# Kernel optimization log

Hardware: AMD Instinct MI355X
Metric: run time of the kernel (lower is better)

The kernel has to match this reference:

```python
import jax, jax.numpy as jnp
import numpy as np

D = 256   # vec_dim
H = 8     # head_num
P = 1024  # patch_num
N = 8     # batch


def setup_inputs() -> dict:
    key = jax.random.key(0)
    ks = jax.random.split(key, 11)
    s = 0.05
    return {
        "inputs": jax.random.normal(ks[0], (N, D, P), dtype=jnp.float32),
        "pos_mat": jax.random.normal(ks[1], (1, H, P, P), dtype=jnp.float32),
        "Wk": jax.random.normal(ks[2], (H * D, D), dtype=jnp.float32) * s,
        "bk": jax.random.normal(ks[3], (H * D,), dtype=jnp.float32) * s,
        "Wq": jax.random.normal(ks[4], (H * D, D), dtype=jnp.float32) * s,
        "bq": jax.random.normal(ks[5], (H * D,), dtype=jnp.float32) * s,
        "Wv": jax.random.normal(ks[6], (H * D, D), dtype=jnp.float32) * s,
        "bv": jax.random.normal(ks[7], (H * D,), dtype=jnp.float32) * s,
        "Wo": jax.random.normal(ks[8], (D, H * D), dtype=jnp.float32) * s,
        "bo": jax.random.normal(ks[9], (D,), dtype=jnp.float32) * s,
    }


def reference(inputs, pos_mat, Wk, bk, Wq, bq, Wv, bv, Wo, bo):
    n, d, p = inputs.shape  # [N, D, P]
    h = Wk.shape[0] // d
    # 1x1 Conv1d == per-position GEMM: [H*D,D] x [N,D,P] -> [N,H*D,P] -> [N,H,D,P]
    k = (jnp.einsum('od,ndp->nop', Wk, inputs) + bk[:, None]).reshape(n, h, d, p)
    q = (jnp.einsum('od,ndp->nop', Wq, inputs) + bq[:, None]).reshape(n, h, d, p)
    v = (jnp.einsum('od,ndp->nop', Wv, inputs) + bv[:, None]).reshape(n, h, d, p)
    # attn[n,h,kpos,qpos] = K^T Q / sqrt(D), shape [N,H,P,P]
    attn = jnp.einsum('nhdk,nhdq->nhkq', k, q) / jnp.sqrt(jnp.asarray(d, inputs.dtype))
    attn = attn + pos_mat
    # NOTE: original uses Softmax(dim=2), i.e. over the KEY axis, not the last dim
    w = jax.nn.softmax(attn, axis=2)
    out = jnp.einsum('nhdk,nhkq->nhdq', v, w).reshape(n, h * d, p)
    return jnp.einsum('oi,nip->nop', Wo, out) + bo[:, None]
```

## Files before the change

kernel.cpp:

```cpp
#include <hip/hip_runtime.h>

typedef __bf16 bf16;
typedef __attribute__((ext_vector_type(8))) __bf16 bf16x8;
typedef __attribute__((ext_vector_type(4))) __bf16 bf16x4;
typedef __attribute__((ext_vector_type(2))) __bf16 bf16x2;
typedef __attribute__((ext_vector_type(4))) float f32x4;

#define MFMA16(a, b, c) __builtin_amdgcn_mfma_f32_16x16x32_bf16(a, b, c, 0, 0, 0)

__device__ __forceinline__ void gload_lds16(const void* g, void* l) {
  __builtin_amdgcn_global_load_lds(
      (const __attribute__((address_space(1))) void*)g,
      (__attribute__((address_space(3))) void*)l, 16, 0, 0);
}

constexpr int NH = 8, DD = 256, PP = 1024;

constexpr size_t WB_YT  = 33554432;
constexpr size_t WB_XB  = 67108864;
constexpr size_t WB_XBT = 71303168;
constexpr size_t WB_MB  = 75497472;
constexpr size_t WB_UB  = 76546048;
constexpr size_t WB_U   = 77594624;
constexpr size_t WB_BP  = 77602816;

constexpr int FL_PT0  = 0;
constexpr int FL_XT0  = 16384;
constexpr int FL_LRED = 0;
constexpr int FL_SZ   = 81920;

#define EXP_SHIFT 4.0f

__global__ __launch_bounds__(256, 1) void msa_mu(
    const float* __restrict__ Wk, const float* __restrict__ Wq,
    const float* __restrict__ Wo, const float* __restrict__ Wv,
    bf16* __restrict__ Mb, bf16* __restrict__ Ub) {
  __shared__ float lds[64 * 65];
  const int t = threadIdx.x;
  const int i0 = (blockIdx.x >> 1) * 64;
  const int jh = blockIdx.x & 1;
  const int h = blockIdx.y;
  const int mode = blockIdx.z;
  const int j0 = (t & 63) * 2 + jh * 128;
  const int ihalf = t >> 6;
  float acc0[16], acc1[16];
#pragma unroll
  for (int r = 0; r < 16; ++r) { acc0[r] = 0.f; acc1[r] = 0.f; }
  const float* __restrict__ W2 = (mode == 0) ? Wq : Wv;
  for (int dhc = 0; dhc < 256; dhc += 64) {
    __syncthreads();
    if (mode == 0) {
#pragma unroll
      for (int s = 0; s < 16; ++s) {
        int f = t + s * 256;
        int dh = f >> 6, ii = f & 63;
        lds[dh * 65 + ii] = Wk[(h * 256 + dhc + dh) * 256 + i0 + ii];
      }
    } else {
#pragma unroll
      for (int s = 0; s < 16; ++s) {
        int f = t + s * 256;
        int oo = f >> 6, dh = f & 63;
        lds[dh * 65 + oo] = Wo[(i0 + oo) * 2048 + h * 256 + dhc + dh];
      }
    }
    __syncthreads();
    for (int dl = 0; dl < 64; ++dl) {
      float2 wv = *reinterpret_cast<const float2*>(&W2[(h * 256 + dhc + dl) * 256 + j0]);
#pragma unroll
      for (int r = 0; r < 16; ++r) {
        float x = lds[dl * 65 + ihalf * 16 + r];
        acc0[r] = fmaf(x, wv.x, acc0[r]);
        acc1[r] = fmaf(x, wv.y, acc1[r]);
      }
    }
  }
  if (mode == 0) {
#pragma unroll
    for (int r = 0; r < 16; ++r) {
      int i = i0 + ihalf * 16 + r;
      bf16x2 v = { (__bf16)(acc0[r] * 0.0625f), (__bf16)(acc1[r] * 0.0625f) };
      *reinterpret_cast<bf16x2*>(&Mb[h * 65536 + i * 256 + j0]) = v;
    }
  } else {
#pragma unroll
    for (int r = 0; r < 16; ++r) {
      int o = i0 + ihalf * 16 + r;
      bf16x2 v = { (__bf16)acc0[r], (__bf16)acc1[r] };
      *reinterpret_cast<bf16x2*>(&Ub[o * 2048 + h * 256 + j0]) = v;
    }
  }
}

__global__ void msa_u(const float* __restrict__ Wk, const float* __restrict__ bq,
                      float* __restrict__ u) {
  __shared__ float bqs[256];
  const int h = blockIdx.x, t = threadIdx.x;
  bqs[t] = bq[h * 256 + t];
  __syncthreads();
  float acc = 0.f;
  for (int dh = 0; dh < 256; ++dh)
    acc = fmaf(Wk[(h * 256 + dh) * 256 + t], bqs[dh], acc);
  u[h * 256 + t] = acc * 0.0625f;
}

__global__ void msa_bp(const float* __restrict__ Wo, const float* __restrict__ bv,
                       const float* __restrict__ bo, float* __restrict__ bp) {
  const int o = blockIdx.x, t = threadIdx.x;
  float acc = 0.f;
  for (int f = t; f < 2048; f += 256)
    acc = fmaf(Wo[o * 2048 + f], bv[f], acc);
#pragma unroll
  for (int m = 32; m >= 1; m >>= 1) acc += __shfl_down(acc, m);
  __shared__ float part[4];
  if ((t & 63) == 0) part[t >> 6] = acc;
  __syncthreads();
  if (t == 0) bp[o] = bo[o] + part[0] + part[1] + part[2] + part[3];
}

__global__ __launch_bounds__(256, 4) void msa_cvtX(
    const float* __restrict__ X, bf16* __restrict__ Xb, bf16* __restrict__ XbT) {
  __shared__ __bf16 tl[64 * 68];
  const int t = threadIdx.x;
  const int p0 = blockIdx.x * 64, d0 = blockIdx.y * 64, n = blockIdx.z;
  const float* __restrict__ Xn = X + (size_t)n * DD * PP;
#pragma unroll
  for (int rr = 0; rr < 4; ++rr) {
    int r = (t >> 4) + rr * 16, c = (t & 15) * 4;
    float4 v = *reinterpret_cast<const float4*>(Xn + (size_t)(d0 + r) * PP + p0 + c);
    bf16x4 pk = { (__bf16)v.x, (__bf16)v.y, (__bf16)v.z, (__bf16)v.w };
    *reinterpret_cast<bf16x4*>(Xb + (size_t)n * DD * PP + (size_t)(d0 + r) * PP + p0 + c) = pk;
    *reinterpret_cast<bf16x4*>(&tl[r * 68 + c]) = pk;
  }
  __syncthreads();
#pragma unroll
  for (int rr = 0; rr < 4; ++rr) {
    int pr = (t >> 4) + rr * 16, dc = (t & 15) * 4;
    bf16x4 pk = { tl[(dc + 0) * 68 + pr], tl[(dc + 1) * 68 + pr],
                  tl[(dc + 2) * 68 + pr], tl[(dc + 3) * 68 + pr] };
    *reinterpret_cast<bf16x4*>(XbT + (size_t)n * PP * DD + (size_t)(p0 + pr) * DD + d0 + dc) = pk;
  }
}

__global__ __launch_bounds__(256, 2) void msa_flash(
    const bf16* __restrict__ XbT, const bf16* __restrict__ Xb,
    const bf16* __restrict__ Mb, const float* __restrict__ u,
    const float* __restrict__ pos, bf16* __restrict__ Yt) {
  extern __shared__ char smc[];
  const int t = threadIdx.x;
  const int lane = t & 63, w = t >> 6;
  const int g = lane >> 4, ln = lane & 15;
  const int kw = w >> 1, qw = w & 1;
  const int qt = blockIdx.x, h = blockIdx.y, n = blockIdx.z;
  const int qg0 = qt * 64, nh = n * 8 + h;
  const bf16* __restrict__ XbTn = XbT + (size_t)n * (PP * DD);
  const bf16* __restrict__ Xbn  = Xb + (size_t)n * (DD * PP);
  const bf16* __restrict__ Mh   = Mb + (size_t)h * (DD * DD);
  const float* __restrict__ posh = pos + (size_t)h * (PP * PP);
  float* lredp = (float*)(smc + FL_LRED);

  const int grl = lane >> 5;
  const int gcb = lane & 31;

  {
    bf16x8 ta[4][8];
#pragma unroll
    for (int mq = 0; mq < 4; ++mq)
#pragma unroll
      for (int s = 0; s < 8; ++s)
        ta[mq][s] = *reinterpret_cast<const bf16x8*>(
            XbTn + (size_t)(qg0 + mq * 16 + ln) * DD + s * 32 + g * 8);
#pragma unroll
    for (int ni = 0; ni < 4; ++ni) {
      const int i_ = w * 64 + ni * 16 + ln;
      bf16x8 tb8[8];
#pragma unroll
      for (int s = 0; s < 8; ++s)
        tb8[s] = *reinterpret_cast<const bf16x8*>(Mh + (size_t)i_ * DD + s * 32 + g * 8);
      const float uv = u[h * 256 + i_];
#pragma unroll
      for (int mq = 0; mq < 4; ++mq) {
        f32x4 acc = {0.f, 0.f, 0.f, 0.f};
#pragma unroll
        for (int s = 0; s < 8; ++s) acc = MFMA16(ta[mq][s], tb8[s], acc);
#pragma unroll
        for (int r = 0; r < 4; ++r) {
          const int q = mq * 16 + 4 * g + r;
          const int addr = FL_XT0 + q * 512 +
              (((w * 8 + ni * 2 + (ln >> 3)) ^ (q & 7)) << 4) + (ln & 7) * 2;
          *reinterpret_cast<__bf16*>(smc + addr) = (__bf16)(acc[r] + uv);
        }
      }
    }
  }
  __syncthreads();

  bf16x8 tb[2][8];
#pragma unroll
  for (int nq = 0; nq < 2; ++nq) {
    const int q_ = qw * 32 + nq * 16 + ln;
#pragma unroll
    for (int s = 0; s < 8; ++s)
      tb[nq][s] = *reinterpret_cast<const bf16x8*>(
          smc + FL_XT0 + q_ * 512 + (((4 * s + g) ^ (q_ & 7)) << 4));
  }
  __syncthreads();

#pragma unroll
  for (int c = 0; c < 8; ++c) {
    const int row = w * 16 + c * 2 + grl;
    const int cbg = gcb ^ (row & 7);
    gload_lds16(XbTn + (size_t)row * DD + cbg * 8,
                smc + FL_XT0 + w * 8192 + c * 1024);
  }
  __syncthreads();

  float lsum[2] = {0.f, 0.f};
  f32x4 yacc[4][4];
#pragma unroll
  for (int a = 0; a < 4; ++a)
#pragma unroll
    for (int b = 0; b < 4; ++b) { f32x4 z = {0.f, 0.f, 0.f, 0.f}; yacc[a][b] = z; }

  for (int kt = 0; kt < 16; ++kt) {
    const int kg0 = kt * 64;
    const int curXT = FL_XT0 + (kt & 1) * 32768;
    const int nxtXT = FL_XT0 + ((kt + 1) & 1) * 32768;
    const int curPT = FL_PT0 + (kt & 1) * 8192;
    if (kt < 15) {
#pragma unroll
      for (int c = 0; c < 8; ++c) {
        const int row = w * 16 + c * 2 + grl;
        const int cbg = gcb ^ (row & 7);
        gload_lds16(XbTn + (size_t)(kg0 + 64 + row) * DD + cbg * 8,
                    smc + nxtXT + w * 8192 + c * 1024);
      }
    }
    float posv[2][2][4];
#pragma unroll
    for (int mt = 0; mt < 2; ++mt)
#pragma unroll
      for (int nq = 0; nq < 2; ++nq) {
        const float* pr = posh + (size_t)(kg0 + kw * 32 + mt * 16 + 4 * g) * PP +
                          qg0 + qw * 32 + nq * 16 + ln;
#pragma unroll
        for (int r = 0; r < 4; ++r) posv[mt][nq][r] = pr[(size_t)r * PP];
      }
    f32x4 sacc[2][2];
#pragma unroll
    for (int a = 0; a < 2; ++a)
#pragma unroll
      for (int b = 0; b < 2; ++b) { f32x4 z = {0.f, 0.f, 0.f, 0.f}; sacc[a][b] = z; }
#pragma unroll
    for (int mt = 0; mt < 2; ++mt) {
      const int row = kw * 32 + mt * 16 + ln;
      bf16x8 af8[8];
#pragma unroll
      for (int s = 0; s < 8; ++s)
        af8[s] = *reinterpret_cast<const bf16x8*>(
            smc + curXT + row * 512 + (((4 * s + g) ^ (row & 7)) << 4));
#pragma unroll
      for (int s = 0; s < 8; ++s)
#pragma unroll
        for (int nq = 0; nq < 2; ++nq)
          sacc[mt][nq] = MFMA16(af8[s], tb[nq][s], sacc[mt][nq]);
    }
#pragma unroll
    for (int mt = 0; mt < 2; ++mt)
#pragma unroll
      for (int nq = 0; nq < 2; ++nq) {
        bf16x4 pk;
#pragma unroll
        for (int r = 0; r < 4; ++r) {
          float e = __expf(sacc[mt][nq][r] + posv[mt][nq][r] - EXP_SHIFT);
          lsum[nq] += e;
          pk[r] = (__bf16)e;
        }
        const int q_ = qw * 32 + nq * 16 + ln;
        *reinterpret_cast<bf16x4*>(smc + curPT + q_ * 128 +
            (((kw * 4 + mt * 2 + (g >> 1)) ^ (q_ & 7)) << 4) + ((g & 1) << 3)) = pk;
      }
    __syncthreads();
#pragma unroll
    for (int ks = 0; ks < 2; ++ks) {
      bf16x8 pa[4], xv[4];
#pragma unroll
      for (int mq = 0; mq < 4; ++mq) {
        const int q_ = mq * 16 + ln;
        pa[mq] = *reinterpret_cast<const bf16x8*>(
            smc + curPT + q_ * 128 + (((4 * ks + g) ^ (q_ & 7)) << 4));
      }
#pragma unroll
      for (int nd = 0; nd < 4; ++nd)
        xv[nd] = *reinterpret_cast<const bf16x8*>(
            Xbn + (size_t)(w * 64 + nd * 16 + ln) * PP + kg0 + ks * 32 + g * 8);
#pragma unroll
      for (int mq = 0; mq < 4; ++mq)
#pragma unroll
        for (int nd = 0; nd < 4; ++nd)
          yacc[mq][nd] = MFMA16(pa[mq], xv[nd], yacc[mq][nd]);
    }
  }

#pragma unroll
  for (int nq = 0; nq < 2; ++nq) {
    lsum[nq] += __shfl_xor(lsum[nq], 16);
    lsum[nq] += __shfl_xor(lsum[nq], 32);
  }
  if (lane < 16) {
#pragma unroll
    for (int nq = 0; nq < 2; ++nq)
      lredp[kw * 64 + qw * 32 + nq * 16 + ln] = lsum[nq];
  }
  __syncthreads();
  bf16* __restrict__ Ytp = Yt + (size_t)nh * (PP * DD);
#pragma unroll
  for (int mq = 0; mq < 4; ++mq) {
    f32x4 l0 = *reinterpret_cast<const f32x4*>(lredp + mq * 16 + 4 * g);
    f32x4 l1 = *reinterpret_cast<const f32x4*>(lredp + 64 + mq * 16 + 4 * g);
    f32x4 inv;
#pragma unroll
    for (int r = 0; r < 4; ++r) inv[r] = 1.0f / (l0[r] + l1[r]);
#pragma unroll
    for (int nd = 0; nd < 4; ++nd)
#pragma unroll
      for (int r = 0; r < 4; ++r)
        Ytp[(size_t)(qg0 + mq * 16 + 4 * g + r) * DD + w * 64 + nd * 16 + ln] =
            (__bf16)(yacc[mq][nd][r] * inv[r]);
  }
}

__global__ __launch_bounds__(256, 3) void msa_final4(
    const bf16* __restrict__ Ub, const bf16* __restrict__ Yt,
    const float* __restrict__ bp, float* __restrict__ out) {
  __shared__ char lsd[49152];
  const int t = threadIdx.x, lane = t & 63, w = t >> 6;
  const int g = lane >> 4, ln = lane & 15;
  const int pw = w & 1, ow = w >> 1;
  const int pb = blockIdx.x * 128, ob = blockIdx.y * 64, n = blockIdx.z;
  const bf16* __restrict__ Ytn = Yt + (size_t)n * 8 * (PP * DD);
  f32x4 acc[2][4];
#pragma unroll
  for (int a = 0; a < 2; ++a)
#pragma unroll
    for (int b = 0; b < 4; ++b) { f32x4 z = {0.f, 0.f, 0.f, 0.f}; acc[a][b] = z; }

  uint4 areg[2], breg[4];
  {
#pragma unroll
    for (int j = 0; j < 2; ++j) {
      int u_ = t + j * 256;
      areg[j] = *reinterpret_cast<const uint4*>(
          Ub + (size_t)(ob + (u_ >> 3)) * 2048 + 0 + (u_ & 7) * 8);
    }
#pragma unroll
    for (int j = 0; j < 4; ++j) {
      int v_ = t + j * 256;
      breg[j] = *reinterpret_cast<const uint4*>(
          Ytn + ((size_t)0 * PP + pb + (v_ >> 3)) * DD + 0 + (v_ & 7) * 8);
    }
#pragma unroll
    for (int j = 0; j < 2; ++j) {
      int u_ = t + j * 256, row = u_ >> 3, cb = u_ & 7;
      *reinterpret_cast<uint4*>(lsd + row * 128 + ((cb ^ (row & 7)) << 4)) = areg[j];
    }
#pragma unroll
    for (int j = 0; j < 4; ++j) {
      int v_ = t + j * 256, row = v_ >> 3, cb = v_ & 7;
      *reinterpret_cast<uint4*>(lsd + 8192 + row * 128 + ((cb ^ (row & 7)) << 4)) = breg[j];
    }
  }
  __syncthreads();

  for (int kc = 0; kc < 32; ++kc) {
    const int cur = (kc & 1) * 24576;
    const int nxt = ((kc + 1) & 1) * 24576;
    if (kc < 31) {
      const int k1 = (kc + 1) * 64, hh = k1 >> 8, dd = k1 & 255;
#pragma unroll
      for (int j = 0; j < 2; ++j) {
        int u_ = t + j * 256;
        areg[j] = *reinterpret_cast<const uint4*>(
            Ub + (size_t)(ob + (u_ >> 3)) * 2048 + k1 + (u_ & 7) * 8);
      }
#pragma unroll
      for (int j = 0; j < 4; ++j) {
        int v_ = t + j * 256;
        breg[j] = *reinterpret_cast<const uint4*>(
            Ytn + ((size_t)hh * PP + pb + (v_ >> 3)) * DD + dd + (v_ & 7) * 8);
      }
    }
#pragma unroll
    for (int ks = 0; ks < 2; ++ks) {
      bf16x8 a[2], b[4];
#pragma unroll
      for (int mo = 0; mo < 2; ++mo) {
        const int row = ow * 32 + mo * 16 + ln;
        a[mo] = *reinterpret_cast<const bf16x8*>(
            lsd + cur + row * 128 + (((4 * ks + g) ^ (row & 7)) << 4));
      }
#pragma unroll
      for (int np = 0; np < 4; ++np) {
        const int row = pw * 64 + np * 16 + ln;
        b[np] = *reinterpret_cast<const bf16x8*>(
            lsd + cur + 8192 + row * 128 + (((4 * ks + g) ^ (row & 7)) << 4));
      }
#pragma unroll
      for (int mo = 0; mo < 2; ++mo)
#pragma unroll
        for (int np = 0; np < 4; ++np) acc[mo][np] = MFMA16(a[mo], b[np], acc[mo][np]);
    }
    if (kc < 31) {
#pragma unroll
      for (int j = 0; j < 2; ++j) {
        int u_ = t + j * 256, row = u_ >> 3, cb = u_ & 7;
        *reinterpret_cast<uint4*>(lsd + nxt + row * 128 + ((cb ^ (row & 7)) << 4)) = areg[j];
      }
#pragma unroll
      for (int j = 0; j < 4; ++j) {
        int v_ = t + j * 256, row = v_ >> 3, cb = v_ & 7;
        *reinterpret_cast<uint4*>(lsd + nxt + 8192 + row * 128 + ((cb ^ (row & 7)) << 4)) = breg[j];
      }
    }
    __syncthreads();
  }

#pragma unroll
  for (int mo = 0; mo < 2; ++mo) {
    f32x4 bv = *reinterpret_cast<const f32x4*>(bp + ob + ow * 32 + mo * 16 + 4 * g);
#pragma unroll
    for (int np = 0; np < 4; ++np)
#pragma unroll
      for (int r = 0; r < 4; ++r) {
        const int o = ob + ow * 32 + mo * 16 + 4 * g + r;
        out[((size_t)n * DD + o) * PP + pb + pw * 64 + np * 16 + ln] =
            acc[mo][np][r] + bv[r];
      }
  }
}

extern "C" void kernel_launch(void* const* d_in, const int* in_sizes, int n_in,
                              void* d_out, int out_size, void* d_ws, size_t ws_size,
                              hipStream_t stream) {
  const float* X   = (const float*)d_in[0];
  const float* pos = (const float*)d_in[1];
  const float* Wk  = (const float*)d_in[2];
  const float* Wq  = (const float*)d_in[4];
  const float* bq  = (const float*)d_in[5];
  const float* Wv  = (const float*)d_in[6];
  const float* bv  = (const float*)d_in[7];
  const float* Wo  = (const float*)d_in[8];
  const float* bo  = (const float*)d_in[9];

  char* ws = (char*)d_ws;
  bf16* Yt  = (bf16*)(ws + WB_YT);
  bf16* Xb  = (bf16*)(ws + WB_XB);
  bf16* XbT = (bf16*)(ws + WB_XBT);
  bf16* Mb  = (bf16*)(ws + WB_MB);
  bf16* Ub  = (bf16*)(ws + WB_UB);
  float* u  = (float*)(ws + WB_U);
  float* bp = (float*)(ws + WB_BP);
  float* out = (float*)d_out;

  hipFuncSetAttribute(reinterpret_cast<const void*>(msa_flash),
                      hipFuncAttributeMaxDynamicSharedMemorySize, FL_SZ);

  msa_cvtX<<<dim3(16, 4, 8), 256, 0, stream>>>(X, Xb, XbT);
  msa_mu<<<dim3(8, 8, 2), 256, 0, stream>>>(Wk, Wq, Wo, Wv, Mb, Ub);
  msa_u<<<8, 256, 0, stream>>>(Wk, bq, u);
  msa_bp<<<256, 256, 0, stream>>>(Wo, bv, bo, bp);
  msa_flash<<<dim3(16, 8, 8), 256, FL_SZ, stream>>>(XbT, Xb, Mb, u, pos, Yt);
  msa_final4<<<dim3(8, 4, 8), 256, 0, stream>>>(Ub, Yt, bp, out);
}
```

Before: 282.5 us.

## Prefetch pos and X loads, add MFMA priority, remap flash grid, split msa_mu

Several separate changes ship together. In the flash kernel the pos_mat tile for the next key tile is prefetched into registers while the current tile computes, and the V-side X loads are hoisted to the top of each iteration. s_setprio raises wave priority around the MFMA blocks. The flash grid becomes 1D with heads innermost, so blocks sharing the same batch's X sit near each other in dispatch order and may reuse it in L2. msa_mu gets twice as many blocks with half the work each; the extra in-flight loads raise register pressure, which could limit the two-blocks-per-CU occupancy.

```diff
diff --git a/kernel.cpp b/kernel.cpp
--- a/kernel.cpp
+++ b/kernel.cpp
@@ -37,15 +37,15 @@
     bf16* __restrict__ Mb, bf16* __restrict__ Ub) {
   __shared__ float lds[64 * 65];
   const int t = threadIdx.x;
-  const int i0 = (blockIdx.x >> 1) * 64;
-  const int jh = blockIdx.x & 1;
+  const int i0 = (blockIdx.x >> 2) * 64;
+  const int jq = blockIdx.x & 3;
   const int h = blockIdx.y;
   const int mode = blockIdx.z;
-  const int j0 = (t & 63) * 2 + jh * 128;
-  const int ihalf = t >> 6;
-  float acc0[16], acc1[16];
-#pragma unroll
-  for (int r = 0; r < 16; ++r) { acc0[r] = 0.f; acc1[r] = 0.f; }
+  const int j0 = (t & 31) * 2 + jq * 64;
+  const int i8 = t >> 5;
+  float acc0[8], acc1[8];
+#pragma unroll
+  for (int r = 0; r < 8; ++r) { acc0[r] = 0.f; acc1[r] = 0.f; }
   const float* __restrict__ W2 = (mode == 0) ? Wq : Wv;
   for (int dhc = 0; dhc < 256; dhc += 64) {
     __syncthreads();
@@ -68,8 +68,8 @@
     for (int dl = 0; dl < 64; ++dl) {
       float2 wv = *reinterpret_cast<const float2*>(&W2[(h * 256 + dhc + dl) * 256 + j0]);
 #pragma unroll
-      for (int r = 0; r < 16; ++r) {
-        float x = lds[dl * 65 + ihalf * 16 + r];
+      for (int r = 0; r < 8; ++r) {
+        float x = lds[dl * 65 + i8 * 8 + r];
         acc0[r] = fmaf(x, wv.x, acc0[r]);
         acc1[r] = fmaf(x, wv.y, acc1[r]);
       }
@@ -77,15 +77,15 @@
   }
   if (mode == 0) {
 #pragma unroll
-    for (int r = 0; r < 16; ++r) {
-      int i = i0 + ihalf * 16 + r;
+    for (int r = 0; r < 8; ++r) {
+      int i = i0 + i8 * 8 + r;
       bf16x2 v = { (__bf16)(acc0[r] * 0.0625f), (__bf16)(acc1[r] * 0.0625f) };
       *reinterpret_cast<bf16x2*>(&Mb[h * 65536 + i * 256 + j0]) = v;
     }
   } else {
 #pragma unroll
-    for (int r = 0; r < 16; ++r) {
-      int o = i0 + ihalf * 16 + r;
+    for (int r = 0; r < 8; ++r) {
+      int o = i0 + i8 * 8 + r;
       bf16x2 v = { (__bf16)acc0[r], (__bf16)acc1[r] };
       *reinterpret_cast<bf16x2*>(&Ub[o * 2048 + h * 256 + j0]) = v;
     }
@@ -151,7 +151,8 @@
   const int lane = t & 63, w = t >> 6;
   const int g = lane >> 4, ln = lane & 15;
   const int kw = w >> 1, qw = w & 1;
-  const int qt = blockIdx.x, h = blockIdx.y, n = blockIdx.z;
+  const int bid = blockIdx.x;
+  const int h = bid & 7, qt = (bid >> 3) & 15, n = bid >> 7;
   const int qg0 = qt * 64, nh = n * 8 + h;
   const bf16* __restrict__ XbTn = XbT + (size_t)n * (PP * DD);
   const bf16* __restrict__ Xbn  = Xb + (size_t)n * (DD * PP);
@@ -213,6 +214,16 @@
     gload_lds16(XbTn + (size_t)row * DD + cbg * 8,
                 smc + FL_XT0 + w * 8192 + c * 1024);
   }
+  float posv[2][2][4];
+#pragma unroll
+  for (int mt = 0; mt < 2; ++mt)
+#pragma unroll
+    for (int nq = 0; nq < 2; ++nq) {
+      const float* pr = posh + (size_t)(kw * 32 + mt * 16 + 4 * g) * PP +
+                        qg0 + qw * 32 + nq * 16 + ln;
+#pragma unroll
+      for (int r = 0; r < 4; ++r) posv[mt][nq][r] = pr[(size_t)r * PP];
+    }
   __syncthreads();
 
   float lsum[2] = {0.f, 0.f};
@@ -236,21 +247,19 @@
                     smc + nxtXT + w * 8192 + c * 1024);
       }
     }
-    float posv[2][2][4];
-#pragma unroll
-    for (int mt = 0; mt < 2; ++mt)
-#pragma unroll
-      for (int nq = 0; nq < 2; ++nq) {
-        const float* pr = posh + (size_t)(kg0 + kw * 32 + mt * 16 + 4 * g) * PP +
-                          qg0 + qw * 32 + nq * 16 + ln;
-#pragma unroll
-        for (int r = 0; r < 4; ++r) posv[mt][nq][r] = pr[(size_t)r * PP];
-      }
+    bf16x8 xv[2][4];
+#pragma unroll
+    for (int ks = 0; ks < 2; ++ks)
+#pragma unroll
+      for (int nd = 0; nd < 4; ++nd)
+        xv[ks][nd] = *reinterpret_cast<const bf16x8*>(
+            Xbn + (size_t)(w * 64 + nd * 16 + ln) * PP + kg0 + ks * 32 + g * 8);
     f32x4 sacc[2][2];
 #pragma unroll
     for (int a = 0; a < 2; ++a)
 #pragma unroll
       for (int b = 0; b < 2; ++b) { f32x4 z = {0.f, 0.f, 0.f, 0.f}; sacc[a][b] = z; }
+    __builtin_amdgcn_s_setprio(1);
 #pragma unroll
     for (int mt = 0; mt < 2; ++mt) {
       const int row = kw * 32 + mt * 16 + ln;
@@ -264,6 +273,19 @@
 #pragma unroll
         for (int nq = 0; nq < 2; ++nq)
           sacc[mt][nq] = MFMA16(af8[s], tb[nq][s], sacc[mt][nq]);
+    }
+    __builtin_amdgcn_s_setprio(0);
+    float posvn[2][2][4];
+    if (kt < 15) {
+#pragma unroll
+      for (int mt = 0; mt < 2; ++mt)
+#pragma unroll
+        for (int nq = 0; nq < 2; ++nq) {
+          const float* pr = posh + (size_t)(kg0 + 64 + kw * 32 + mt * 16 + 4 * g) * PP +
+                            qg0 + qw * 32 + nq * 16 + ln;
+#pragma unroll
+          for (int r = 0; r < 4; ++r) posvn[mt][nq][r] = pr[(size_t)r * PP];
+        }
     }
 #pragma unroll
     for (int mt = 0; mt < 2; ++mt)
@@ -281,9 +303,10 @@
             (((kw * 4 + mt * 2 + (g >> 1)) ^ (q_ & 7)) << 4) + ((g & 1) << 3)) = pk;
       }
     __syncthreads();
+    __builtin_amdgcn_s_setprio(1);
 #pragma unroll
     for (int ks = 0; ks < 2; ++ks) {
-      bf16x8 pa[4], xv[4];
+      bf16x8 pa[4];
 #pragma unroll
       for (int mq = 0; mq < 4; ++mq) {
         const int q_ = mq * 16 + ln;
@@ -291,14 +314,19 @@
             smc + curPT + q_ * 128 + (((4 * ks + g) ^ (q_ & 7)) << 4));
       }
 #pragma unroll
-      for (int nd = 0; nd < 4; ++nd)
-        xv[nd] = *reinterpret_cast<const bf16x8*>(
-            Xbn + (size_t)(w * 64 + nd * 16 + ln) * PP + kg0 + ks * 32 + g * 8);
-#pragma unroll
       for (int mq = 0; mq < 4; ++mq)
 #pragma unroll
         for (int nd = 0; nd < 4; ++nd)
-          yacc[mq][nd] = MFMA16(pa[mq], xv[nd], yacc[mq][nd]);
+          yacc[mq][nd] = MFMA16(pa[mq], xv[ks][nd], yacc[mq][nd]);
+    }
+    __builtin_amdgcn_s_setprio(0);
+    if (kt < 15) {
+#pragma unroll
+      for (int mt = 0; mt < 2; ++mt)
+#pragma unroll
+        for (int nq = 0; nq < 2; ++nq)
+#pragma unroll
+          for (int r = 0; r < 4; ++r) posv[mt][nq][r] = posvn[mt][nq][r];
     }
   }
 
@@ -466,9 +494,9 @@
                       hipFuncAttributeMaxDynamicSharedMemorySize, FL_SZ);
 
   msa_cvtX<<<dim3(16, 4, 8), 256, 0, stream>>>(X, Xb, XbT);
-  msa_mu<<<dim3(8, 8, 2), 256, 0, stream>>>(Wk, Wq, Wo, Wv, Mb, Ub);
+  msa_mu<<<dim3(16, 8, 2), 256, 0, stream>>>(Wk, Wq, Wo, Wv, Mb, Ub);
   msa_u<<<8, 256, 0, stream>>>(Wk, bq, u);
   msa_bp<<<256, 256, 0, stream>>>(Wo, bv, bo, bp);
-  msa_flash<<<dim3(16, 8, 8), 256, FL_SZ, stream>>>(XbT, Xb, Mb, u, pos, Yt);
+  msa_flash<<<1024, 256, FL_SZ, stream>>>(XbT, Xb, Mb, u, pos, Yt);
   msa_final4<<<dim3(8, 4, 8), 256, 0, stream>>>(Ub, Yt, bp, out);
 }
```

New measurement: 286.5 us. Within noise of the previous version (+1.4%).
